# Performance work log

Measured on AMD Instinct MI355X. Metric: run time of the kernel, lower is better.

## Reference

```python
import jax, jax.numpy as jnp
import numpy as np

B, L, M = 8, 200, 4
S, D, Q = 100, 128, 10000
NRG = NPC = NAC = 20
F = 4                       # len(forget_window)+1
NTOT = F * (NRG + NPC + NAC + 15)   # 300


def setup_inputs():
    key = jax.random.key(0)
    ks = jax.random.split(key, 40)
    ri = lambda k, sh, hi: jax.random.randint(k, sh, 0, hi)
    rn = lambda k, sh: jax.random.normal(k, sh, jnp.float32) * 0.02

    def make_c(k1, k2):
        # distinct concept ids per (b,l) row (matches typical data; makes scatter deterministic)
        base = jax.random.randint(k1, (B, L, 1), 0, S)
        cc = (base + jnp.arange(M)) % S
        mask = jax.random.uniform(k2, (B, L, M)) < 0.2
        return jnp.where(mask, -1, cc)

    inp = dict(
        q=ri(ks[0], (B, L), Q),
        c=make_c(ks[1], ks[2]),
        shift_q=ri(ks[3], (B, L), Q),
        shift_c=make_c(ks[4], ks[5]),
        r=ri(ks[6], (B, L), 2),
        rgaps=ri(ks[7], (B, L, M), NRG),
        pcounts=ri(ks[8], (B, L, M, F), NPC),
        acounts=ri(ks[9], (B, L, M, F), NAC),
        shft_rgaps=ri(ks[10], (B, L, M), NRG),
        shft_pcounts=ri(ks[11], (B, L, M, F), NPC),
        shft_acounts=ri(ks[12], (B, L, M, F), NAC),
        E_skill=rn(ks[13], (S, D)),
        E_question=rn(ks[14], (Q, D)),
        E_response=rn(ks[15], (2, D)),
        wih_in=rn(ks[16], (4 * D, D)), whh_in=rn(ks[17], (4 * D, D)),
        bih_in=rn(ks[18], (4 * D,)), bhh_in=rn(ks[19], (4 * D,)),
        wih_fg=rn(ks[20], (4 * D, D)), whh_fg=rn(ks[21], (4 * D, D)),
        bih_fg=rn(ks[22], (4 * D,)), bhh_fg=rn(ks[23], (4 * D,)),
        W_l2=rn(ks[24], (3 * D, D)), b_l2=rn(ks[25], (D,)),
        W_l3=rn(ks[26], (2 * D, D)), b_l3=rn(ks[27], (D,)),
        W_fc3=rn(ks[28], (2 * D, 1)), b_fc3=rn(ks[29], (1,)),
        W_fc4=rn(ks[30], (2 * D, D)), b_fc4=rn(ks[31], (D,)),
        W_fc5=rn(ks[32], (2 * D, D)), b_fc5=rn(ks[33], (D,)),
        W_cemb=rn(ks[34], (NTOT, D)),                      # cemb, no bias
        W_pre=rn(ks[35], (S * (D + NTOT), D)), b_pre=rn(ks[36], (D,)),
    )
    return inp


def _lstm(x, wih, whh, bih, bhh):
    # Faithful to source: torch LSTM default is seq-first and the module passes
    # [B,L,D] unchanged, so recurrence runs over axis 0 of the given tensor.
    H = whh.shape[1]

    def step(carry, xt):
        h, cs = carry
        g = xt @ wih.T + h @ whh.T + bih + bhh
        i, f, gg, o = jnp.split(g, 4, axis=-1)
        cs = jax.nn.sigmoid(f) * cs + jax.nn.sigmoid(i) * jnp.tanh(gg)
        h = jax.nn.sigmoid(o) * jnp.tanh(cs)
        return (h, cs), h

    z = jnp.zeros((x.shape[1], H), x.dtype)
    _, hs = jax.lax.scan(step, (z, z), x)
    return hs


def _concept_true(c, E_skill):
    # eye(S+1)[c][..., :-1] summed over M: -1 maps to an all-zero row
    cv1 = jax.nn.one_hot(c, S).sum(-2)              # [B,L,S]
    return cv1[..., None] * E_skill[None, None]     # [B,L,S,D]


def _attention(q, ct):
    scores = jnp.einsum('bld,blsd->bls', q, ct) / jnp.asarray(np.sqrt(D), q.dtype)
    w = jax.nn.softmax(scores, axis=-1)
    return jnp.einsum('bls,blsd->bld', w, ct)


def _forget(c, rg, pc, ac, E_skill, W_cemb, W_pre, b_pre):
    rg4 = jnp.broadcast_to(rg[..., None], (B, L, M, F))
    fv1 = jnp.concatenate([
        jax.nn.one_hot(rg4, NRG + 5).reshape(B, L, M, -1),
        jax.nn.one_hot(pc, NPC + 5).reshape(B, L, M, -1),
        jax.nn.one_hot(ac, NAC + 5).reshape(B, L, M, -1)], -1)   # [B,L,M,NTOT]
    # vectorized masked scatter replacing the triple Python loop: -1 -> dummy row S
    tgt = jnp.where(c < 0, S, c)
    bi = jnp.arange(B)[:, None, None]
    li = jnp.arange(L)[None, :, None]
    fv2 = jnp.zeros((B, L, S + 1, NTOT), fv1.dtype).at[bi, li, tgt].set(fv1)[:, :, :S]
    Cct = fv2 @ W_cemb                                           # [B,L,S,D]
    theta = _concept_true(c, E_skill) * Cct
    theta = jnp.concatenate([theta, fv2], -1).reshape(B, L, -1)  # [B,L,S*(D+NTOT)]
    return theta @ W_pre + b_pre


def reference(q, c, shift_q, shift_c, r, rgaps, pcounts, acounts,
              shft_rgaps, shft_pcounts, shft_acounts,
              E_skill, E_question, E_response,
              wih_in, whh_in, bih_in, bhh_in,
              wih_fg, whh_fg, bih_fg, bhh_fg,
              W_l2, b_l2, W_l3, b_l3, W_fc3, b_fc3,
              W_fc4, b_fc4, W_fc5, b_fc5, W_cemb, W_pre, b_pre):
    emb_q = E_question[q]
    emb_r = E_response[r]
    att = _attention(emb_q, _concept_true(c, E_skill))
    xemb = jnp.concatenate([emb_q, emb_r, att], -1) @ W_l2 + b_l2
    input_h = _lstm(xemb, wih_in, whh_in, bih_in, bhh_in)        # dropout = eval identity
    fh = _forget(c, rgaps, pcounts, acounts, E_skill, W_cemb, W_pre, b_pre)
    forget_h = _lstm(fh, wih_fg, whh_fg, bih_fg, bhh_fg)
    shift = E_question[shift_q]
    s_att = _attention(shift, _concept_true(shift_c, E_skill))
    shift = jnp.concatenate([shift, s_att], -1) @ W_l3 + b_l3
    shift_forget = _forget(shift_c, shft_rgaps, shft_pcounts, shft_acounts,
                           E_skill, W_cemb, W_pre, b_pre)
    x1 = jax.nn.relu(jnp.concatenate([shift, input_h], -1) @ W_fc4 + b_fc4)
    x2 = jax.nn.relu(jnp.concatenate([shift_forget, forget_h], -1) @ W_fc5 + b_fc5)
    y = jax.nn.sigmoid(jnp.concatenate([x1, x2], -1) @ W_fc3 + b_fc3)
    return y.squeeze(-1)   # [B,L]
```

## Files before the change

kernel.cpp:

```cpp
#include <hip/hip_runtime.h>
#include <hip/hip_bf16.h>
#include <math.h>

#define BB   8
#define LL   200
#define MM   4
#define SS   100
#define DD   128
#define FF   4
#define NT   300
#define ROWS (BB*LL)
#define JT2  64

#define NB_TR  128
#define NB_TP  500
#define NB_AT  800
#define NB_PJ  400
#define NB_FH  1600

__device__ __forceinline__ float sigf(float x){ return 1.f/(1.f+expf(-x)); }

__device__ __forceinline__ unsigned short f2bf(float x){
    unsigned int u = __float_as_uint(x);
    unsigned int r = (u + 0x7FFFu + ((u >> 16) & 1u)) >> 16;
    return (unsigned short)r;
}
__device__ __forceinline__ float bf2f(unsigned short v){
    return __uint_as_float(((unsigned int)v) << 16);
}

__global__ void __launch_bounds__(256) k_stage1(
    const float* __restrict__ wih_in, const float* __restrict__ wih_fg,
    const float* __restrict__ whh_in, const float* __restrict__ whh_fg,
    float* __restrict__ wT_in, float* __restrict__ wT_fg,
    float* __restrict__ whhT_in, float* __restrict__ whhT_fg,
    const float* __restrict__ Es, const float* __restrict__ Wc,
    const float* __restrict__ Wp, unsigned short* __restrict__ T16,
    const int* __restrict__ q,  const int* __restrict__ c,
    const int* __restrict__ sq, const int* __restrict__ sc,
    const float* __restrict__ Eq,
    float* __restrict__ att0, float* __restrict__ att1)
{
    __shared__ float WcL[JT2][128];
    int b   = blockIdx.x;
    int tid = threadIdx.x;

    if (b < NB_TR) {
        for (int e = b*256 + tid; e < 4*65536; e += NB_TR*256) {
            int mat = e >> 16, o = e & 65535;
            int k = o >> 9, g = o & 511;
            const float* src = (mat==0)?wih_in:(mat==1)?wih_fg:(mat==2)?whh_in:whh_fg;
            float*       dst = (mat==0)?wT_in:(mat==1)?wT_fg:(mat==2)?whhT_in:whhT_fg;
            dst[o] = src[g*128 + k];
        }
        return;
    }
    if (b < NB_TR + NB_TP) {
        int bb2 = b - NB_TR;
        int s  = bb2 / 5;
        int jc = bb2 - s*5;
        int j0 = jc * JT2;
        const float* es = Es + s*128;
        for (int idx = tid; idx < JT2*128; idx += 256) {
            int jj = idx >> 7, d = idx & 127;
            int j = j0 + jj;
            WcL[jj][d] = (j < NT) ? Wc[j*128 + d] * es[d] : 0.f;
        }
        __syncthreads();

        const float*  wp  = Wp + (size_t)s*428*128;
        const float4* wp4 = (const float4*)wp;
        int tq = tid & 31;
        int jg = tid >> 5;
        float4 acc[8];
        #pragma unroll
        for (int j = 0; j < 8; j++) acc[j] = make_float4(0.f,0.f,0.f,0.f);

        for (int d4 = 0; d4 < 128; d4 += 4) {
            float4 wv[4];
            #pragma unroll
            for (int u = 0; u < 4; u++) wv[u] = wp4[(d4+u)*32 + tq];
            float4 wc[8];
            #pragma unroll
            for (int j = 0; j < 8; j++)
                wc[j] = *(const float4*)&WcL[jg*8 + j][d4];
            #pragma unroll
            for (int u = 0; u < 4; u++) {
                float4 wpv = wv[u];
                #pragma unroll
                for (int j = 0; j < 8; j++) {
                    float w = (u==0)?wc[j].x:(u==1)?wc[j].y:(u==2)?wc[j].z:wc[j].w;
                    acc[j].x += w * wpv.x;
                    acc[j].y += w * wpv.y;
                    acc[j].z += w * wpv.z;
                    acc[j].w += w * wpv.w;
                }
            }
        }

        const float4* wpe4 = (const float4*)(wp + 128*128);
        ushort4* T4 = (ushort4*)T16;
        #pragma unroll
        for (int j = 0; j < 8; j++) {
            int jj = j0 + jg*8 + j;
            if (jj < NT) {
                float4 bv = wpe4[(size_t)jj*32 + tq];
                ushort4 st;
                st.x = f2bf(acc[j].x + bv.x);
                st.y = f2bf(acc[j].y + bv.y);
                st.z = f2bf(acc[j].z + bv.z);
                st.w = f2bf(acc[j].w + bv.w);
                T4[((size_t)s*NT + jj)*32 + tq] = st;
            }
        }
        return;
    }
    {
        int wv   = tid >> 6;
        int lane = tid & 63;
        int task = (b - NB_TR - NB_TP)*4 + wv;
        int row   = task >> 1;
        int which = task & 1;
        const int* qq = which ? sq : q;
        const int* cc = which ? sc : c;
        float* out = which ? att1 : att0;

        size_t qb = (size_t)qq[row]*128;
        float eq0 = Eq[qb + lane];
        float eq1 = Eq[qb + 64 + lane];
        int   s[4];
        float es0[4], es1[4], d[4];
        #pragma unroll
        for (int m = 0; m < 4; m++) {
            s[m]  = cc[row*4 + m];
            es0[m] = (s[m] >= 0) ? Es[s[m]*128 + lane]      : 0.f;
            es1[m] = (s[m] >= 0) ? Es[s[m]*128 + 64 + lane] : 0.f;
            d[m] = eq0*es0[m] + eq1*es1[m];
        }
        #pragma unroll
        for (int off = 32; off > 0; off >>= 1) {
            #pragma unroll
            for (int m = 0; m < 4; m++) d[m] += __shfl_xor(d[m], off);
        }
        const float inv = 0.08838834764831845f;
        int   nact = 0;
        float mx = 0.f;
        #pragma unroll
        for (int m = 0; m < 4; m++) {
            d[m] *= inv;
            if (s[m] >= 0) { nact++; mx = fmaxf(mx, d[m]); }
        }
        float Z = (float)(SS - nact) * expf(-mx);
        float w[4];
        #pragma unroll
        for (int m = 0; m < 4; m++) {
            w[m] = (s[m] >= 0) ? expf(d[m] - mx) : 0.f;
            Z += w[m];
        }
        float a0 = 0.f, a1 = 0.f;
        #pragma unroll
        for (int m = 0; m < 4; m++) {
            float ww = w[m]/Z;
            a0 += ww * es0[m];
            a1 += ww * es1[m];
        }
        out[row*128 + lane]      = a0;
        out[row*128 + 64 + lane] = a1;
    }
}

__global__ void __launch_bounds__(256) k_stage2(
    const int* __restrict__ q, const int* __restrict__ r, const int* __restrict__ sq,
    const float* __restrict__ Eq, const float* __restrict__ Er,
    const float* __restrict__ att, const float* __restrict__ satt,
    const float* __restrict__ Wl2, const float* __restrict__ bl2,
    const float* __restrict__ Wl3, const float* __restrict__ bl3,
    float* __restrict__ xemb, float* __restrict__ shiftx,
    const int* __restrict__ c,  const int* __restrict__ rg,
    const int* __restrict__ pc, const int* __restrict__ ac,
    const int* __restrict__ sc, const int* __restrict__ srg,
    const int* __restrict__ spc,const int* __restrict__ sac,
    const unsigned short* __restrict__ T16, const float* __restrict__ bpre,
    float* __restrict__ fh0, float* __restrict__ fh1)
{
    __shared__ float xs1[4][384];
    __shared__ float xs2[4][256];
    __shared__ float part[2][4][128];
    int b   = blockIdx.x;
    int tid = threadIdx.x;

    if (b < NB_PJ) {
        int r0 = b*4;
        for (int e = tid; e < 4*384; e += 256) {
            int i = e / 384, pos = e - i*384;
            int row = r0 + i;
            float v;
            if (pos < 128)      v = Eq[(size_t)q[row]*128 + pos];
            else if (pos < 256) v = Er[r[row]*128 + (pos-128)];
            else                v = att[row*128 + (pos-256)];
            xs1[i][pos] = v;
        }
        for (int e = tid; e < 4*256; e += 256) {
            int i = e >> 8, pos = e & 255;
            int row = r0 + i;
            xs2[i][pos] = (pos < 128) ? Eq[(size_t)sq[row]*128 + pos]
                                      : satt[row*128 + (pos-128)];
        }
        __syncthreads();

        int kg  = tid >> 7;
        int col = tid & 127;
        {
            float acc[4];
            #pragma unroll
            for (int i = 0; i < 4; i++) acc[i] = 0.f;
            int k0 = kg*192;
            for (int kb = 0; kb < 192; kb += 8) {
                float wb[8];
                #pragma unroll
                for (int u = 0; u < 8; u++) wb[u] = Wl2[(k0+kb+u)*128 + col];
                #pragma unroll
                for (int u = 0; u < 8; u++) {
                    #pragma unroll
                    for (int i = 0; i < 4; i++) acc[i] += xs1[i][k0+kb+u]*wb[u];
                }
            }
            #pragma unroll
            for (int i = 0; i < 4; i++) part[kg][i][col] = acc[i];
        }
        __syncthreads();
        for (int e = tid; e < 512; e += 256) {
            int i = e >> 7, cc2 = e & 127;
            xemb[(r0+i)*128 + cc2] = bl2[cc2] + part[0][i][cc2] + part[1][i][cc2];
        }
        __syncthreads();
        {
            float acc[4];
            #pragma unroll
            for (int i = 0; i < 4; i++) acc[i] = 0.f;
            int k0 = kg*128;
            for (int kb = 0; kb < 128; kb += 8) {
                float wb[8];
                #pragma unroll
                for (int u = 0; u < 8; u++) wb[u] = Wl3[(k0+kb+u)*128 + col];
                #pragma unroll
                for (int u = 0; u < 8; u++) {
                    #pragma unroll
                    for (int i = 0; i < 4; i++) acc[i] += xs2[i][k0+kb+u]*wb[u];
                }
            }
            #pragma unroll
            for (int i = 0; i < 4; i++) part[kg][i][col] = acc[i];
        }
        __syncthreads();
        for (int e = tid; e < 512; e += 256) {
            int i = e >> 7, cc2 = e & 127;
            shiftx[(r0+i)*128 + cc2] = bl3[cc2] + part[0][i][cc2] + part[1][i][cc2];
        }
        return;
    }
    {
        int u     = (b - NB_PJ)*2 + (tid >> 7);
        int which = u & 1;
        int row   = u >> 1;
        int t     = tid & 127;
        const int* C  = which ? sc  : c;
        const int* RG = which ? srg : rg;
        const int* PC = which ? spc : pc;
        const int* AC = which ? sac : ac;
        float* out = which ? fh1 : fh0;

        float acc = bpre[t];
        for (int m = 0; m < 4; m++) {
            int s = C[row*4 + m];
            if (s < 0) continue;
            int rgv = RG[row*4 + m];
            const unsigned short* Ts = T16 + (size_t)s*NT*128;
            #pragma unroll
            for (int f = 0; f < 4; f++) {
                int j1 = f*25 + rgv;
                int j2 = 100 + f*25 + PC[(row*4+m)*4 + f];
                int j3 = 200 + f*25 + AC[(row*4+m)*4 + f];
                acc += bf2f(Ts[j1*128 + t]) + bf2f(Ts[j2*128 + t]) + bf2f(Ts[j3*128 + t]);
            }
        }
        out[row*128 + t] = acc;
    }
}

__global__ void __launch_bounds__(512) k_lstm(
    const float* __restrict__ xemb, const float* __restrict__ fh,
    const float* __restrict__ wT_in, const float* __restrict__ wT_fg,
    const float* __restrict__ whhT_in, const float* __restrict__ whhT_fg,
    const float* __restrict__ bih_in, const float* __restrict__ bhh_in,
    const float* __restrict__ bih_fg, const float* __restrict__ bhh_fg,
    float* __restrict__ h_in_out, float* __restrict__ h_fg_out)
{
    int which = blockIdx.y;
    const float* X  = which ? fh      : xemb;
    const float* WI = which ? wT_fg   : wT_in;
    const float* WH = which ? whhT_fg : whhT_in;
    const float* B1 = which ? bih_fg  : bih_in;
    const float* B2 = which ? bhh_fg  : bhh_in;
    float* OUT = which ? h_fg_out : h_in_out;

    int l0  = blockIdx.x;
    int tid = threadIdx.x;

    __shared__ float xr[8][128];
    __shared__ float gb[8][512];
    __shared__ float h[128], cs[128], gl[512];

    for (int e = tid; e < 1024; e += 512) {
        int t = e >> 7, d = e & 127;
        xr[t][d] = X[(size_t)(t*200 + l0)*128 + d];
    }
    if (tid < 128) { h[tid] = 0.f; cs[tid] = 0.f; }
    __syncthreads();

    float bb = B1[tid] + B2[tid];
    {
        float a[8];
        #pragma unroll
        for (int i = 0; i < 8; i++) a[i] = bb;
        for (int kb = 0; kb < 128; kb += 8) {
            float wv[8];
            #pragma unroll
            for (int u = 0; u < 8; u++) wv[u] = WI[(kb+u)*512 + tid];
            #pragma unroll
            for (int u = 0; u < 8; u++) {
                #pragma unroll
                for (int i = 0; i < 8; i++) a[i] += xr[i][kb+u]*wv[u];
            }
        }
        #pragma unroll
        for (int i = 0; i < 8; i++) gb[i][tid] = a[i];
    }

    float w[128];
    #pragma unroll
    for (int k = 0; k < 128; k++) w[k] = WH[k*512 + tid];
    __syncthreads();

    for (int t = 0; t < 8; t++) {
        float a0 = gb[t][tid];
        #pragma unroll
        for (int k = 0; k < 128; k++) a0 += h[k]*w[k];
        gl[tid] = a0;
        __syncthreads();
        if (tid < 128) {
            float gi = gl[tid], gf = gl[128+tid], gg = gl[256+tid], go = gl[384+tid];
            float cn = sigf(gf)*cs[tid] + sigf(gi)*tanhf(gg);
            float hn = sigf(go)*tanhf(cn);
            cs[tid] = cn;
            h[tid]  = hn;
            OUT[(size_t)(t*200 + l0)*128 + tid] = hn;
        }
        __syncthreads();
    }
}

__global__ void __launch_bounds__(256) k_final(
    const float* __restrict__ shiftx, const float* __restrict__ h_in,
    const float* __restrict__ fh_shift, const float* __restrict__ h_fg,
    const float* __restrict__ Wfc4, const float* __restrict__ bfc4,
    const float* __restrict__ Wfc5, const float* __restrict__ bfc5,
    const float* __restrict__ Wfc3, const float* __restrict__ bfc3,
    float* __restrict__ out)
{
    int r0  = blockIdx.x * 4;
    int tid = threadIdx.x;
    int kg  = tid >> 7;
    int col = tid & 127;
    __shared__ float xa[4][256], xb[4][256];
    __shared__ float part[2][4][128];

    for (int e = tid; e < 4*256; e += 256) {
        int i = e >> 8, pos = e & 255;
        int row = r0 + i;
        xa[i][pos] = (pos < 128) ? shiftx[row*128 + pos]   : h_in[row*128 + pos-128];
        xb[i][pos] = (pos < 128) ? fh_shift[row*128 + pos] : h_fg[row*128 + pos-128];
    }
    __syncthreads();

    float acc4[4], acc5[4];
    #pragma unroll
    for (int i = 0; i < 4; i++) { acc4[i] = 0.f; acc5[i] = 0.f; }
    int k0 = kg * 128;
    for (int kb = 0; kb < 128; kb += 8) {
        float w4[8], w5[8];
        #pragma unroll
        for (int u = 0; u < 8; u++) {
            w4[u] = Wfc4[(k0+kb+u)*128 + col];
            w5[u] = Wfc5[(k0+kb+u)*128 + col];
        }
        #pragma unroll
        for (int u = 0; u < 8; u++) {
            int k = k0 + kb + u;
            #pragma unroll
            for (int i = 0; i < 4; i++) {
                acc4[i] += xa[i][k] * w4[u];
                acc5[i] += xb[i][k] * w5[u];
            }
        }
    }

    #pragma unroll
    for (int i = 0; i < 4; i++) part[kg][i][col] = acc4[i];
    __syncthreads();
    float x1r[2];
    #pragma unroll
    for (int j = 0; j < 2; j++) {
        int e = tid + 256*j;
        int i = e >> 7, cc2 = e & 127;
        x1r[j] = fmaxf(part[0][i][cc2] + part[1][i][cc2] + bfc4[cc2], 0.f);
    }
    __syncthreads();
    #pragma unroll
    for (int i = 0; i < 4; i++) part[kg][i][col] = acc5[i];
    __syncthreads();
    float x2r[2];
    #pragma unroll
    for (int j = 0; j < 2; j++) {
        int e = tid + 256*j;
        int i = e >> 7, cc2 = e & 127;
        x2r[j] = fmaxf(part[0][i][cc2] + part[1][i][cc2] + bfc5[cc2], 0.f);
    }
    __syncthreads();

    float* cont = &part[0][0][0];
    #pragma unroll
    for (int j = 0; j < 2; j++) {
        int e = tid + 256*j;
        int i = e >> 7, cc2 = e & 127;
        cont[i*128 + cc2] = x1r[j]*Wfc3[cc2] + x2r[j]*Wfc3[128 + cc2];
    }
    __syncthreads();
    int wv = tid >> 6, lane = tid & 63;
    float sum = cont[wv*128 + lane] + cont[wv*128 + lane + 64];
    #pragma unroll
    for (int off = 32; off > 0; off >>= 1) sum += __shfl_xor(sum, off);
    if (lane == 0) out[r0 + wv] = 1.f/(1.f + expf(-(sum + bfc3[0])));
}

extern "C" void kernel_launch(void* const* d_in, const int* in_sizes, int n_in,
                              void* d_out, int out_size, void* d_ws, size_t ws_size,
                              hipStream_t stream)
{
    const int*   q      = (const int*)d_in[0];
    const int*   c      = (const int*)d_in[1];
    const int*   sq     = (const int*)d_in[2];
    const int*   sc     = (const int*)d_in[3];
    const int*   r      = (const int*)d_in[4];
    const int*   rg     = (const int*)d_in[5];
    const int*   pc     = (const int*)d_in[6];
    const int*   ac     = (const int*)d_in[7];
    const int*   srg    = (const int*)d_in[8];
    const int*   spc    = (const int*)d_in[9];
    const int*   sac    = (const int*)d_in[10];
    const float* Es     = (const float*)d_in[11];
    const float* Eq     = (const float*)d_in[12];
    const float* Er     = (const float*)d_in[13];
    const float* wih_in = (const float*)d_in[14];
    const float* whh_in = (const float*)d_in[15];
    const float* bih_in = (const float*)d_in[16];
    const float* bhh_in = (const float*)d_in[17];
    const float* wih_fg = (const float*)d_in[18];
    const float* whh_fg = (const float*)d_in[19];
    const float* bih_fg = (const float*)d_in[20];
    const float* bhh_fg = (const float*)d_in[21];
    const float* Wl2    = (const float*)d_in[22];
    const float* bl2    = (const float*)d_in[23];
    const float* Wl3    = (const float*)d_in[24];
    const float* bl3    = (const float*)d_in[25];
    const float* Wfc3   = (const float*)d_in[26];
    const float* bfc3   = (const float*)d_in[27];
    const float* Wfc4   = (const float*)d_in[28];
    const float* bfc4   = (const float*)d_in[29];
    const float* Wfc5   = (const float*)d_in[30];
    const float* bfc5   = (const float*)d_in[31];
    const float* Wc     = (const float*)d_in[32];
    const float* Wp     = (const float*)d_in[33];
    const float* bpre   = (const float*)d_in[34];

    float* W = (float*)d_ws;
    unsigned short* T16 = (unsigned short*)W;  W += 100*NT*128/2;
    float* att     = W;  W += ROWS*128;
    float* satt    = W;  W += ROWS*128;
    float* xemb    = W;  W += ROWS*128;
    float* shiftx  = W;  W += ROWS*128;
    float* fh0     = W;  W += ROWS*128;
    float* fh1     = W;  W += ROWS*128;
    float* wT_in   = W;  W += 512*128;
    float* wT_fg   = W;  W += 512*128;
    float* whhT_in = W;  W += 512*128;
    float* whhT_fg = W;  W += 512*128;
    float* h_in    = W;  W += ROWS*128;
    float* h_fg    = W;  W += ROWS*128;

    hipLaunchKernelGGL(k_stage1, dim3(NB_TR + NB_TP + NB_AT), dim3(256), 0, stream,
        wih_in, wih_fg, whh_in, whh_fg, wT_in, wT_fg, whhT_in, whhT_fg,
        Es, Wc, Wp, T16,
        q, c, sq, sc, Eq, att, satt);

    hipLaunchKernelGGL(k_stage2, dim3(NB_PJ + NB_FH), dim3(256), 0, stream,
        q, r, sq, Eq, Er, att, satt, Wl2, bl2, Wl3, bl3, xemb, shiftx,
        c, rg, pc, ac, sc, srg, spc, sac, T16, bpre, fh0, fh1);

    hipLaunchKernelGGL(k_lstm, dim3(200, 2), dim3(512), 0, stream,
        xemb, fh0, wT_in, wT_fg, whhT_in, whhT_fg,
        bih_in, bhh_in, bih_fg, bhh_fg, h_in, h_fg);

    hipLaunchKernelGGL(k_final, dim3(400), dim3(256), 0, stream,
        shiftx, h_in, fh1, h_fg, Wfc4, bfc4, Wfc5, bfc5, Wfc3, bfc3, (float*)d_out);
}
```

Baseline: 246.1 us.

## Split LSTM input projection into separate gates kernel and batch recurrence over two columns

Moves the input-to-hidden projection out of the recurrent kernel into a standalone k_gates kernel that writes precomputed gate pre-activations to a workspace buffer, using a paired weight layout. The recurrent kernel now handles two independent sequences per block, keeps Whh in LDS as packed bf16 instead of 128 fp32 registers per thread, and broadcasts h through readlane. The aim is to cut register pressure, halve the number of blocks that each load Whh, and shorten the serial critical path. In exchange it adds a kernel launch, a 2x ROWS*512 gate buffer round trip through global memory, and bf16 rounding of the recurrent weights.

New measurement: 251.2 us. +2.1%, slower.

```diff
diff --git a/kernel.cpp b/kernel.cpp
--- a/kernel.cpp
+++ b/kernel.cpp
@@ -20,19 +20,23 @@
 
 __device__ __forceinline__ float sigf(float x){ return 1.f/(1.f+expf(-x)); }
 
-__device__ __forceinline__ unsigned short f2bf(float x){
+__device__ __forceinline__ unsigned int f2bf(float x){
     unsigned int u = __float_as_uint(x);
-    unsigned int r = (u + 0x7FFFu + ((u >> 16) & 1u)) >> 16;
-    return (unsigned short)r;
+    return (u + 0x7FFFu + ((u >> 16) & 1u)) >> 16;
 }
 __device__ __forceinline__ float bf2f(unsigned short v){
     return __uint_as_float(((unsigned int)v) << 16);
+}
+__device__ __forceinline__ float bflo(unsigned int w){ return __uint_as_float(w << 16); }
+__device__ __forceinline__ float bfhi(unsigned int w){ return __uint_as_float(w & 0xffff0000u); }
+__device__ __forceinline__ float rdlane(float v, int k){
+    return __int_as_float(__builtin_amdgcn_readlane(__float_as_int(v), k));
 }
 
 __global__ void __launch_bounds__(256) k_stage1(
     const float* __restrict__ wih_in, const float* __restrict__ wih_fg,
     const float* __restrict__ whh_in, const float* __restrict__ whh_fg,
-    float* __restrict__ wT_in, float* __restrict__ wT_fg,
+    float* __restrict__ wP_in, float* __restrict__ wP_fg,
     float* __restrict__ whhT_in, float* __restrict__ whhT_fg,
     const float* __restrict__ Es, const float* __restrict__ Wc,
     const float* __restrict__ Wp, unsigned short* __restrict__ T16,
@@ -48,10 +52,15 @@
     if (b < NB_TR) {
         for (int e = b*256 + tid; e < 4*65536; e += NB_TR*256) {
             int mat = e >> 16, o = e & 65535;
-            int k = o >> 9, g = o & 511;
             const float* src = (mat==0)?wih_in:(mat==1)?wih_fg:(mat==2)?whh_in:whh_fg;
-            float*       dst = (mat==0)?wT_in:(mat==1)?wT_fg:(mat==2)?whhT_in:whhT_fg;
-            dst[o] = src[g*128 + k];
+            float*       dst = (mat==0)?wP_in:(mat==1)?wP_fg:(mat==2)?whhT_in:whhT_fg;
+            if (mat < 2) {
+                int cc = o & 1, t2 = o >> 1, pp = t2 & 255, k = t2 >> 8;
+                dst[o] = src[(pp + 256*cc)*128 + k];
+            } else {
+                int k = o >> 9, g = o & 511;
+                dst[o] = src[g*128 + k];
+            }
         }
         return;
     }
@@ -106,10 +115,10 @@
             if (jj < NT) {
                 float4 bv = wpe4[(size_t)jj*32 + tq];
                 ushort4 st;
-                st.x = f2bf(acc[j].x + bv.x);
-                st.y = f2bf(acc[j].y + bv.y);
-                st.z = f2bf(acc[j].z + bv.z);
-                st.w = f2bf(acc[j].w + bv.w);
+                st.x = (unsigned short)f2bf(acc[j].x + bv.x);
+                st.y = (unsigned short)f2bf(acc[j].y + bv.y);
+                st.z = (unsigned short)f2bf(acc[j].z + bv.z);
+                st.w = (unsigned short)f2bf(acc[j].w + bv.w);
                 T4[((size_t)s*NT + jj)*32 + tq] = st;
             }
         }
@@ -288,73 +297,127 @@
     }
 }
 
-__global__ void __launch_bounds__(512) k_lstm(
+__global__ void __launch_bounds__(256) k_gates(
     const float* __restrict__ xemb, const float* __restrict__ fh,
-    const float* __restrict__ wT_in, const float* __restrict__ wT_fg,
-    const float* __restrict__ whhT_in, const float* __restrict__ whhT_fg,
+    const float* __restrict__ wP_in, const float* __restrict__ wP_fg,
     const float* __restrict__ bih_in, const float* __restrict__ bhh_in,
     const float* __restrict__ bih_fg, const float* __restrict__ bhh_fg,
+    float* __restrict__ g_in, float* __restrict__ g_fg)
+{
+    int which = blockIdx.y;
+    const float*  X   = which ? fh : xemb;
+    const float2* Wp2 = (const float2*)(which ? wP_fg : wP_in);
+    const float*  b1  = which ? bih_fg : bih_in;
+    const float*  b2  = which ? bhh_fg : bhh_in;
+    float* G = which ? g_fg : g_in;
+
+    int r0  = blockIdx.x * 8;
+    int tid = threadIdx.x;
+    __shared__ float xl[8][128];
+    for (int e = tid; e < 8*128; e += 256)
+        xl[e>>7][e&127] = X[(size_t)r0*128 + e];
+    __syncthreads();
+
+    int p = tid;
+    float a0[8], a1[8];
+    #pragma unroll
+    for (int i = 0; i < 8; i++) { a0[i] = 0.f; a1[i] = 0.f; }
+    for (int kb = 0; kb < 128; kb += 8) {
+        float2 wbuf[8];
+        #pragma unroll
+        for (int u = 0; u < 8; u++) wbuf[u] = Wp2[(kb+u)*256 + p];
+        #pragma unroll
+        for (int u = 0; u < 8; u++) {
+            #pragma unroll
+            for (int i = 0; i < 8; i++) {
+                float xv = xl[i][kb+u];
+                a0[i] += xv * wbuf[u].x;
+                a1[i] += xv * wbuf[u].y;
+            }
+        }
+    }
+    float bb0 = b1[p] + b2[p];
+    float bb1 = b1[p+256] + b2[p+256];
+    #pragma unroll
+    for (int i = 0; i < 8; i++) {
+        G[(size_t)(r0+i)*512 + p]       = a0[i] + bb0;
+        G[(size_t)(r0+i)*512 + p + 256] = a1[i] + bb1;
+    }
+}
+
+__global__ void __launch_bounds__(512) k_lstm(
+    const float* __restrict__ g_in, const float* __restrict__ g_fg,
+    const float* __restrict__ whhT_in, const float* __restrict__ whhT_fg,
     float* __restrict__ h_in_out, float* __restrict__ h_fg_out)
 {
     int which = blockIdx.y;
-    const float* X  = which ? fh      : xemb;
-    const float* WI = which ? wT_fg   : wT_in;
+    const float* GX = which ? g_fg    : g_in;
     const float* WH = which ? whhT_fg : whhT_in;
-    const float* B1 = which ? bih_fg  : bih_in;
-    const float* B2 = which ? bhh_fg  : bhh_in;
     float* OUT = which ? h_fg_out : h_in_out;
 
-    int l0  = blockIdx.x;
-    int tid = threadIdx.x;
-
-    __shared__ float xr[8][128];
-    __shared__ float gb[8][512];
-    __shared__ float h[128], cs[128], gl[512];
-
-    for (int e = tid; e < 1024; e += 512) {
-        int t = e >> 7, d = e & 127;
-        xr[t][d] = X[(size_t)(t*200 + l0)*128 + d];
-    }
-    if (tid < 128) { h[tid] = 0.f; cs[tid] = 0.f; }
-    __syncthreads();
-
-    float bb = B1[tid] + B2[tid];
-    {
-        float a[8];
-        #pragma unroll
-        for (int i = 0; i < 8; i++) a[i] = bb;
-        for (int kb = 0; kb < 128; kb += 8) {
-            float wv[8];
-            #pragma unroll
-            for (int u = 0; u < 8; u++) wv[u] = WI[(kb+u)*512 + tid];
-            #pragma unroll
-            for (int u = 0; u < 8; u++) {
-                #pragma unroll
-                for (int i = 0; i < 8; i++) a[i] += xr[i][kb+u]*wv[u];
-            }
-        }
-        #pragma unroll
-        for (int i = 0; i < 8; i++) gb[i][tid] = a[i];
-    }
-
-    float w[128];
-    #pragma unroll
-    for (int k = 0; k < 128; k++) w[k] = WH[k*512 + tid];
-    __syncthreads();
-
+    int l0   = blockIdx.x * 2;
+    int tid  = threadIdx.x;
+    int lane = tid & 63;
+
+    __shared__ unsigned int WHb[64*512];
+    __shared__ float hL[2][128], csL[2][128], gl[2][512];
+
+    uint2* WH64w = (uint2*)WHb;
+    for (int e = tid; e < 16384; e += 512) {
+        int p = e & 511, qq = e >> 9;
+        unsigned w0 = f2bf(WH[(4*qq+0)*512+p]) | (f2bf(WH[(4*qq+1)*512+p]) << 16);
+        unsigned w1 = f2bf(WH[(4*qq+2)*512+p]) | (f2bf(WH[(4*qq+3)*512+p]) << 16);
+        WH64w[e] = make_uint2(w0, w1);
+    }
+    if (tid < 256) {
+        int rr = tid >> 7, d = tid & 127;
+        hL[rr][d] = 0.f; csL[rr][d] = 0.f;
+    }
+    __syncthreads();
+
+    const uint2* WH64 = (const uint2*)WHb;
     for (int t = 0; t < 8; t++) {
-        float a0 = gb[t][tid];
-        #pragma unroll
-        for (int k = 0; k < 128; k++) a0 += h[k]*w[k];
-        gl[tid] = a0;
-        __syncthreads();
-        if (tid < 128) {
-            float gi = gl[tid], gf = gl[128+tid], gg = gl[256+tid], go = gl[384+tid];
-            float cn = sigf(gf)*cs[tid] + sigf(gi)*tanhf(gg);
+        float h0lo = hL[0][lane], h0hi = hL[0][lane+64];
+        float h1lo = hL[1][lane], h1hi = hL[1][lane+64];
+        float a0 = GX[(size_t)(t*200 + l0)*512 + tid];
+        float a1 = GX[(size_t)(t*200 + l0 + 1)*512 + tid];
+        #pragma unroll
+        for (int qq = 0; qq < 16; qq++) {
+            uint2 w2 = WH64[qq*512 + tid];
+            float wa = bflo(w2.x), wb = bfhi(w2.x);
+            float wc = bflo(w2.y), wd = bfhi(w2.y);
+            int k = qq*4;
+            float p0 = rdlane(h0lo,k), p1 = rdlane(h0lo,k+1),
+                  p2 = rdlane(h0lo,k+2), p3 = rdlane(h0lo,k+3);
+            float s0 = rdlane(h1lo,k), s1 = rdlane(h1lo,k+1),
+                  s2 = rdlane(h1lo,k+2), s3 = rdlane(h1lo,k+3);
+            a0 += p0*wa + p1*wb + p2*wc + p3*wd;
+            a1 += s0*wa + s1*wb + s2*wc + s3*wd;
+        }
+        #pragma unroll
+        for (int qq = 16; qq < 32; qq++) {
+            uint2 w2 = WH64[qq*512 + tid];
+            float wa = bflo(w2.x), wb = bfhi(w2.x);
+            float wc = bflo(w2.y), wd = bfhi(w2.y);
+            int k = qq*4 - 64;
+            float p0 = rdlane(h0hi,k), p1 = rdlane(h0hi,k+1),
+                  p2 = rdlane(h0hi,k+2), p3 = rdlane(h0hi,k+3);
+            float s0 = rdlane(h1hi,k), s1 = rdlane(h1hi,k+1),
+                  s2 = rdlane(h1hi,k+2), s3 = rdlane(h1hi,k+3);
+            a0 += p0*wa + p1*wb + p2*wc + p3*wd;
+            a1 += s0*wa + s1*wb + s2*wc + s3*wd;
+        }
+        gl[0][tid] = a0;
+        gl[1][tid] = a1;
+        __syncthreads();
+        if (tid < 256) {
+            int rr = tid >> 7, d = tid & 127;
+            float gi = gl[rr][d], gf = gl[rr][128+d], gg = gl[rr][256+d], go = gl[rr][384+d];
+            float cn = sigf(gf)*csL[rr][d] + sigf(gi)*tanhf(gg);
             float hn = sigf(go)*tanhf(cn);
-            cs[tid] = cn;
-            h[tid]  = hn;
-            OUT[(size_t)(t*200 + l0)*128 + tid] = hn;
+            csL[rr][d] = cn;
+            hL[rr][d]  = hn;
+            OUT[(size_t)(t*200 + l0 + rr)*128 + d] = hn;
         }
         __syncthreads();
     }
@@ -491,15 +554,17 @@
     float* shiftx  = W;  W += ROWS*128;
     float* fh0     = W;  W += ROWS*128;
     float* fh1     = W;  W += ROWS*128;
-    float* wT_in   = W;  W += 512*128;
-    float* wT_fg   = W;  W += 512*128;
+    float* wP_in   = W;  W += 512*128;
+    float* wP_fg   = W;  W += 512*128;
     float* whhT_in = W;  W += 512*128;
     float* whhT_fg = W;  W += 512*128;
+    float* g_in    = W;  W += ROWS*512;
+    float* g_fg    = W;  W += ROWS*512;
     float* h_in    = W;  W += ROWS*128;
     float* h_fg    = W;  W += ROWS*128;
 
     hipLaunchKernelGGL(k_stage1, dim3(NB_TR + NB_TP + NB_AT), dim3(256), 0, stream,
-        wih_in, wih_fg, whh_in, whh_fg, wT_in, wT_fg, whhT_in, whhT_fg,
+        wih_in, wih_fg, whh_in, whh_fg, wP_in, wP_fg, whhT_in, whhT_fg,
         Es, Wc, Wp, T16,
         q, c, sq, sc, Eq, att, satt);
 
@@ -507,9 +572,11 @@
         q, r, sq, Eq, Er, att, satt, Wl2, bl2, Wl3, bl3, xemb, shiftx,
         c, rg, pc, ac, sc, srg, spc, sac, T16, bpre, fh0, fh1);
 
-    hipLaunchKernelGGL(k_lstm, dim3(200, 2), dim3(512), 0, stream,
-        xemb, fh0, wT_in, wT_fg, whhT_in, whhT_fg,
-        bih_in, bhh_in, bih_fg, bhh_fg, h_in, h_fg);
+    hipLaunchKernelGGL(k_gates, dim3(200, 2), dim3(256), 0, stream,
+        xemb, fh0, wP_in, wP_fg, bih_in, bhh_in, bih_fg, bhh_fg, g_in, g_fg);
+
+    hipLaunchKernelGGL(k_lstm, dim3(100, 2), dim3(512), 0, stream,
+        g_in, g_fg, whhT_in, whhT_fg, h_in, h_fg);
 
     hipLaunchKernelGGL(k_final, dim3(400), dim3(256), 0, stream,
         shiftx, h_in, fh1, h_fg, Wfc4, bfc4, Wfc5, bfc5, Wfc3, bfc3, (float*)d_out);
```
